# Kernel optimization log

Hardware: AMD Instinct MI355X
Metric: run time of the kernel (lower is better)

## Reference

```python
import jax, jax.numpy as jnp
import numpy as np

EPS = 1e-05
NUM_DOMAINS = 8  # num_source_domains


def setup_inputs() -> dict:
    key = jax.random.key(0)
    kx, kd = jax.random.split(key)
    B, C, H, W = 64, 256, 32, 128
    x = jax.random.normal(kx, (B, C, H, W), dtype=jnp.float32)
    # 1-based domain ids in [1, NUM_DOMAINS], one per sample
    domain_ids = jax.random.randint(kd, (B,), 0, NUM_DOMAINS) + 1
    weight = jnp.ones((C,), dtype=jnp.float32)
    bias = jnp.zeros((C,), dtype=jnp.float32)
    return {"x": x, "weight": weight, "bias": bias, "domain_ids": domain_ids}


def reference(x, weight, bias, domain_ids):
    """Training-mode per-domain branch of GoldenSubjectDualStatisticsBatchNorm2d:
    for each domain group, compute biased mean/var over (N_g, H, W) per channel,
    normalize that group's samples with its own stats, apply shared affine.
    Vectorized with segment_sum instead of the torch per-domain Python loop."""
    B, C, H, W = x.shape
    idx = domain_ids - 1  # 0-based segment ids, [B]

    # per-sample spatial sums: [B, C]
    s = jnp.sum(x, axis=(2, 3))
    sq = jnp.sum(x * x, axis=(2, 3))

    # per-domain sums and element counts
    S = jax.ops.segment_sum(s, idx, num_segments=NUM_DOMAINS)   # [D, C]
    SQ = jax.ops.segment_sum(sq, idx, num_segments=NUM_DOMAINS)  # [D, C]
    n = jax.ops.segment_sum(jnp.ones((B,), x.dtype), idx, num_segments=NUM_DOMAINS)
    cnt = jnp.maximum(n * (H * W), 1.0)[:, None]  # [D, 1]; guard empty domains

    mean = S / cnt                      # [D, C]
    var = SQ / cnt - mean * mean        # biased var (unbiased=False)

    m = mean[idx][:, :, None, None]     # gather per-sample stats -> [B, C, 1, 1]
    v = var[idx][:, :, None, None]
    y = (x - m) / jnp.sqrt(v + EPS)
    return y * weight[None, :, None, None] + bias[None, :, None, None]
```

## Files before the change

### kernel.cpp

```cpp
#include <hip/hip_runtime.h>

#define EPS 1e-5f
#define NDOM 8
#define NB 64
#define NC 256
#define NH 32
#define NW 128
#define HW (NH * NW)

__global__ __launch_bounds__(256) void stats_kernel(
    const float* __restrict__ x, const int* __restrict__ dom,
    float* __restrict__ S, float* __restrict__ SQ) {
    const int bc = blockIdx.x;
    const int b = bc / NC;
    const int c = bc % NC;

    const float4* xp = (const float4*)(x + (size_t)bc * HW);
    float s = 0.f, sq = 0.f;
    for (int i = threadIdx.x; i < HW / 4; i += 256) {
        float4 v = xp[i];
        s  += v.x + v.y + v.z + v.w;
        sq += v.x * v.x + v.y * v.y + v.z * v.z + v.w * v.w;
    }
    for (int off = 32; off > 0; off >>= 1) {
        s  += __shfl_down(s, off, 64);
        sq += __shfl_down(sq, off, 64);
    }
    __shared__ float ls[4], lsq[4];
    const int lane = threadIdx.x & 63;
    const int wave = threadIdx.x >> 6;
    if (lane == 0) { ls[wave] = s; lsq[wave] = sq; }
    __syncthreads();
    if (threadIdx.x == 0) {
        float ts  = ls[0] + ls[1] + ls[2] + ls[3];
        float tsq = lsq[0] + lsq[1] + lsq[2] + lsq[3];
        const int d = dom[b] - 1;
        atomicAdd(&S[d * NC + c], ts);
        atomicAdd(&SQ[d * NC + c], tsq);
    }
}

__global__ __launch_bounds__(256) void norm_kernel(
    const float* __restrict__ x, const float* __restrict__ wgt,
    const float* __restrict__ bia, const int* __restrict__ dom,
    const float* __restrict__ S, const float* __restrict__ SQ,
    float* __restrict__ out) {
    const int bc = blockIdx.x;
    const int b = bc / NC;
    const int c = bc % NC;

    __shared__ float sh_scale, sh_shift;
    if (threadIdx.x == 0) {
        const int d = dom[b] - 1;
        int n = 0;
        for (int i = 0; i < NB; ++i) n += (dom[i] - 1 == d) ? 1 : 0;
        const float cnt   = fmaxf((float)n * (float)HW, 1.0f);
        const float mean  = S[d * NC + c] / cnt;
        const float var   = SQ[d * NC + c] / cnt - mean * mean;
        const float inv   = rsqrtf(var + EPS);
        const float scale = wgt[c] * inv;
        sh_scale = scale;
        sh_shift = bia[c] - mean * scale;
    }
    __syncthreads();
    const float scale = sh_scale;
    const float shift = sh_shift;

    const float4* xp = (const float4*)(x + (size_t)bc * HW);
    float4*       op = (float4*)(out + (size_t)bc * HW);
    for (int i = threadIdx.x; i < HW / 4; i += 256) {
        float4 v = xp[i];
        v.x = v.x * scale + shift;
        v.y = v.y * scale + shift;
        v.z = v.z * scale + shift;
        v.w = v.w * scale + shift;
        op[i] = v;
    }
}

extern "C" void kernel_launch(void* const* d_in, const int* in_sizes, int n_in,
                              void* d_out, int out_size, void* d_ws, size_t ws_size,
                              hipStream_t stream) {
    const float* x   = (const float*)d_in[0];
    const float* wgt = (const float*)d_in[1];
    const float* bia = (const float*)d_in[2];
    const int*   dom = (const int*)d_in[3];
    float* out = (float*)d_out;

    float* S  = (float*)d_ws;
    float* SQ = S + NDOM * NC;

    hipMemsetAsync(d_ws, 0, 2 * NDOM * NC * sizeof(float), stream);

    stats_kernel<<<NB * NC, 256, 0, stream>>>(x, dom, S, SQ);
    norm_kernel<<<NB * NC, 256, 0, stream>>>(x, wgt, bia, dom, S, SQ, out);
}
```

Baseline: 485.1 us.

## Split stats into partials+finalize, reverse norm order, nontemporal stores

```diff
diff --git a/kernel.cpp b/kernel.cpp
--- a/kernel.cpp
+++ b/kernel.cpp
@@ -8,17 +8,18 @@
 #define NW 128
 #define HW (NH * NW)
 
-__global__ __launch_bounds__(256) void stats_kernel(
-    const float* __restrict__ x, const int* __restrict__ dom,
-    float* __restrict__ S, float* __restrict__ SQ) {
+typedef float vfloat4 __attribute__((ext_vector_type(4)));
+
+
+__global__ __launch_bounds__(256) void row_stats(
+    const float* __restrict__ x, float2* __restrict__ partial) {
     const int bc = blockIdx.x;
-    const int b = bc / NC;
-    const int c = bc % NC;
+    const vfloat4* xp = (const vfloat4*)(x + (size_t)bc * HW);
 
-    const float4* xp = (const float4*)(x + (size_t)bc * HW);
     float s = 0.f, sq = 0.f;
-    for (int i = threadIdx.x; i < HW / 4; i += 256) {
-        float4 v = xp[i];
+#pragma unroll
+    for (int k = 0; k < 4; ++k) {
+        vfloat4 v = xp[threadIdx.x + k * 256];
         s  += v.x + v.y + v.z + v.w;
         sq += v.x * v.x + v.y * v.y + v.z * v.z + v.w * v.w;
     }
@@ -32,49 +33,59 @@
     if (lane == 0) { ls[wave] = s; lsq[wave] = sq; }
     __syncthreads();
     if (threadIdx.x == 0) {
-        float ts  = ls[0] + ls[1] + ls[2] + ls[3];
-        float tsq = lsq[0] + lsq[1] + lsq[2] + lsq[3];
-        const int d = dom[b] - 1;
-        atomicAdd(&S[d * NC + c], ts);
-        atomicAdd(&SQ[d * NC + c], tsq);
+        partial[bc] = make_float2(ls[0] + ls[1] + ls[2] + ls[3],
+                                  lsq[0] + lsq[1] + lsq[2] + lsq[3]);
     }
 }
 
+__global__ __launch_bounds__(NC) void finalize_stats(
+    const float2* __restrict__ partial, const int* __restrict__ dom,
+    const float* __restrict__ wgt, const float* __restrict__ bia,
+    float2* __restrict__ scale_shift) {
+    const int d = blockIdx.x;
+    const int c = threadIdx.x;
+
+    float S = 0.f, SQ = 0.f;
+    int n = 0;
+    for (int b = 0; b < NB; ++b) {
+        if (dom[b] - 1 == d) {
+            float2 p = partial[b * NC + c];
+            S += p.x;
+            SQ += p.y;
+            ++n;
+        }
+    }
+    const float cnt   = fmaxf((float)n * (float)HW, 1.0f);
+    const float mean  = S / cnt;
+    const float var   = SQ / cnt - mean * mean;
+    const float inv   = rsqrtf(var + EPS);
+    const float scale = wgt[c] * inv;
+    scale_shift[d * NC + c] = make_float2(scale, bia[c] - mean * scale);
+}
+
 __global__ __launch_bounds__(256) void norm_kernel(
-    const float* __restrict__ x, const float* __restrict__ wgt,
-    const float* __restrict__ bia, const int* __restrict__ dom,
-    const float* __restrict__ S, const float* __restrict__ SQ,
-    float* __restrict__ out) {
-    const int bc = blockIdx.x;
+    const float* __restrict__ x, const int* __restrict__ dom,
+    const float2* __restrict__ scale_shift, float* __restrict__ out) {
+    const int bc = NB * NC - 1 - blockIdx.x;
     const int b = bc / NC;
     const int c = bc % NC;
 
-    __shared__ float sh_scale, sh_shift;
-    if (threadIdx.x == 0) {
-        const int d = dom[b] - 1;
-        int n = 0;
-        for (int i = 0; i < NB; ++i) n += (dom[i] - 1 == d) ? 1 : 0;
-        const float cnt   = fmaxf((float)n * (float)HW, 1.0f);
-        const float mean  = S[d * NC + c] / cnt;
-        const float var   = SQ[d * NC + c] / cnt - mean * mean;
-        const float inv   = rsqrtf(var + EPS);
-        const float scale = wgt[c] * inv;
-        sh_scale = scale;
-        sh_shift = bia[c] - mean * scale;
-    }
-    __syncthreads();
-    const float scale = sh_scale;
-    const float shift = sh_shift;
+    const int d = dom[b] - 1;
+    const float2 ss = scale_shift[d * NC + c];
+    const float scale = ss.x;
+    const float shift = ss.y;
 
-    const float4* xp = (const float4*)(x + (size_t)bc * HW);
-    float4*       op = (float4*)(out + (size_t)bc * HW);
-    for (int i = threadIdx.x; i < HW / 4; i += 256) {
-        float4 v = xp[i];
+    const vfloat4* xp = (const vfloat4*)(x + (size_t)bc * HW);
+    vfloat4*       op = (vfloat4*)(out + (size_t)bc * HW);
+#pragma unroll
+    for (int k = 0; k < 4; ++k) {
+        const int i = threadIdx.x + k * 256;
+        vfloat4 v = xp[i];
         v.x = v.x * scale + shift;
         v.y = v.y * scale + shift;
         v.z = v.z * scale + shift;
         v.w = v.w * scale + shift;
-        op[i] = v;
+        __builtin_nontemporal_store(v, &op[i]);
     }
 }
 
@@ -87,11 +98,10 @@
     const int*   dom = (const int*)d_in[3];
     float* out = (float*)d_out;
 
-    float* S  = (float*)d_ws;
-    float* SQ = S + NDOM * NC;
+    float2* partial     = (float2*)d_ws;
+    float2* scale_shift = partial + NB * NC;
 
-    hipMemsetAsync(d_ws, 0, 2 * NDOM * NC * sizeof(float), stream);
-
-    stats_kernel<<<NB * NC, 256, 0, stream>>>(x, dom, S, SQ);
-    norm_kernel<<<NB * NC, 256, 0, stream>>>(x, wgt, bia, dom, S, SQ, out);
+    row_stats<<<NB * NC, 256, 0, stream>>>(x, partial);
+    finalize_stats<<<NDOM, NC, 0, stream>>>(partial, dom, wgt, bia, scale_shift);
+    norm_kernel<<<NB * NC, 256, 0, stream>>>(x, dom, scale_shift, out);
 }
```

Measured after the change: 475.8 us. About the same (-1.9%).
